# Kernel tuning notes

Hardware: AMD Instinct MI355X
Metric: run time of the kernel (lower is better)

The kernel has to match this reference:

```python
import jax, jax.numpy as jnp
import numpy as np


def setup_inputs() -> dict:
    key = jax.random.key(0)
    x = jax.random.normal(key, (32, 512, 32, 32), dtype=jnp.float32)
    return {"x": x}


def reference(x):
    B, C, H, W = x.shape
    # [B, HW, C]
    x_v = x.reshape(B, C, H * W).transpose(0, 2, 1)
    # channel means over spatial positions, detached in original (no grad path)
    x_m = jax.lax.stop_gradient(x_v.mean(axis=1))  # [B, C]
    # pairwise squared-diff score: score[b, i, j] = -(x_m[b, j] - x_m[b, i])**2
    score = -(x_m[:, None, :] - x_m[:, :, None]) ** 2  # [B, C, C]
    attn = jax.nn.softmax(score, axis=1)  # normalize over first channel axis
    # out[b, s, j] = sum_k x_v[b, s, k] * attn[b, k, j]
    out = jnp.einsum("bsk,bkj->bsj", x_v, attn)  # [B, HW, C]
    out = out.transpose(0, 2, 1).reshape(B, C, H, W)
    return jax.nn.relu(x + 0.1 * out)
```

## Files before the change

### kernel.cpp

```cpp
#include <hip/hip_runtime.h>
#include <hip/hip_bf16.h>


typedef __bf16 bf16x8 __attribute__((ext_vector_type(8)));
typedef float floatx4 __attribute__((ext_vector_type(4)));

__device__ __forceinline__ void async_cp16(const void* gsrc, void* ldst) {
    __builtin_amdgcn_global_load_lds(
        (const __attribute__((address_space(1))) unsigned int*)gsrc,
        (__attribute__((address_space(3))) unsigned int*)ldst,
        16, 0, 0);
}

__global__ __launch_bounds__(256) void mean_kernel(const float* __restrict__ x,
                                                   float* __restrict__ xm) {
    int row  = blockIdx.x * 4 + (threadIdx.x >> 6);
    int lane = threadIdx.x & 63;
    const float4* p = (const float4*)(x + (size_t)row * 1024);
    float s = 0.0f;
#pragma unroll
    for (int i = 0; i < 4; i++) {
        float4 v = p[lane + i * 64];
        s += v.x + v.y + v.z + v.w;
    }
#pragma unroll
    for (int off = 32; off; off >>= 1) s += __shfl_down(s, off);
    if (lane == 0) xm[row] = s * (1.0f / 1024.0f);
}

__global__ __launch_bounds__(256) void attn_kernel(const float* __restrict__ xm,
                                                   __bf16* __restrict__ attnT) {
    int gw   = blockIdx.x * 4 + (threadIdx.x >> 6);
    int b    = gw >> 9;
    int j    = gw & 511;
    int lane = threadIdx.x & 63;
    const float* m = xm + b * 512;
    float mj = m[j];
    float e[8];
    float s = 0.0f;
#pragma unroll
    for (int i = 0; i < 8; i++) {
        float d = mj - m[lane + i * 64];
        e[i] = __expf(-d * d);
        s += e[i];
    }
#pragma unroll
    for (int off = 32; off; off >>= 1) s += __shfl_xor(s, off);
    float inv = 1.0f / s;
    __bf16* o = attnT + (size_t)gw * 512;
#pragma unroll
    for (int i = 0; i < 8; i++) o[lane + i * 64] = (__bf16)(e[i] * inv);
}

__global__ __launch_bounds__(256, 3) void gemm_kernel(const __bf16* __restrict__ attnT,
                                                      const float* __restrict__ x,
                                                      float* __restrict__ out) {
    int b  = blockIdx.z;
    int m0 = blockIdx.y * 128;
    int n0 = blockIdx.x * 128;
    const __bf16* Ab = attnT + (size_t)b * 512 * 512 + (size_t)m0 * 512;
    const float*  xb = x + (size_t)b * 512 * 1024;

    __shared__ __bf16 As[2][128][32];
    __shared__ __bf16 Bs[128][64];

    int tid  = threadIdx.x;
    int wave = tid >> 6, lane = tid & 63;
    int wr = wave >> 1, wc = wave & 1;
    int quad = lane >> 4, l16 = lane & 15;

    int ko = tid >> 5;
    int sq = tid & 31;

    floatx4 acc[4][4];
#pragma unroll
    for (int i = 0; i < 4; i++)
#pragma unroll
        for (int j = 0; j < 4; j++) acc[i][j] = (floatx4){0.f, 0.f, 0.f, 0.f};

    for (int k0 = 0; k0 < 512; k0 += 64) {
#pragma unroll
        for (int i = 0; i < 4; i++) {
            int q = tid + i * 256;
            int ulow = q & 3, r = (q >> 2) & 127, p = q >> 9;
            async_cp16(Ab + (size_t)r * 512 + k0 + p * 32 + ulow * 8,
                       (char*)&As[0][0][0] + (size_t)q * 16);
        }
        float4 f[8];
#pragma unroll
        for (int kk = 0; kk < 8; kk++)
            f[kk] = *(const float4*)&xb[(size_t)(k0 + ko * 8 + kk) * 1024 + n0 + sq * 4];
#pragma unroll
        for (int j = 0; j < 4; j++) {
            int s = sq * 4 + j;
            bf16x8 w;
            w[0] = (__bf16)f[0].x; w[1] = (__bf16)f[1].x;
            w[2] = (__bf16)f[2].x; w[3] = (__bf16)f[3].x;
            w[4] = (__bf16)f[4].x; w[5] = (__bf16)f[5].x;
            w[6] = (__bf16)f[6].x; w[7] = (__bf16)f[7].x;
            const float* fp = (const float*)&f[0];
#pragma unroll
            for (int kk = 0; kk < 8; kk++) w[kk] = (__bf16)fp[kk * 4 + j];
            int u = ko ^ (((s >> 2) ^ s) & 7);
            *(bf16x8*)&Bs[s][u * 8] = w;
        }
        __syncthreads();
#pragma unroll
        for (int ks = 0; ks < 2; ks++) {
            bf16x8 af[4], bfv[4];
#pragma unroll
            for (int mi = 0; mi < 4; mi++)
                af[mi] = *(bf16x8*)&As[ks][wr * 64 + mi * 16 + l16][quad * 8];
#pragma unroll
            for (int ni = 0; ni < 4; ni++) {
                int n = wc * 64 + ni * 16 + l16;
                int u = (ks * 4 + quad) ^ (((n >> 2) ^ n) & 7);
                bfv[ni] = *(bf16x8*)&Bs[n][u * 8];
            }
#pragma unroll
            for (int mi = 0; mi < 4; mi++)
#pragma unroll
                for (int ni = 0; ni < 4; ni++)
                    acc[mi][ni] = __builtin_amdgcn_mfma_f32_16x16x32_bf16(
                        af[mi], bfv[ni], acc[mi][ni], 0, 0, 0);
        }
        __syncthreads();
    }

    float* ob = out + (size_t)b * 512 * 1024;
#pragma unroll
    for (int mi = 0; mi < 4; mi++)
#pragma unroll
        for (int r = 0; r < 4; r++) {
            int j = m0 + wr * 64 + mi * 16 + quad * 4 + r;
#pragma unroll
            for (int ni = 0; ni < 4; ni++) {
                int s = n0 + wc * 64 + ni * 16 + l16;
                float v = xb[(size_t)j * 1024 + s] + 0.1f * acc[mi][ni][r];
                ob[(size_t)j * 1024 + s] = fmaxf(v, 0.0f);
            }
        }
}

extern "C" void kernel_launch(void* const* d_in, const int* in_sizes, int n_in,
                              void* d_out, int out_size, void* d_ws, size_t ws_size,
                              hipStream_t stream) {
    const float* x = (const float*)d_in[0];
    float* out = (float*)d_out;
    char* ws = (char*)d_ws;
    float*  xm    = (float*)ws;
    __bf16* attnT = (__bf16*)(ws + (64 << 10));

    mean_kernel<<<4096, 256, 0, stream>>>(x, xm);
    attn_kernel<<<4096, 256, 0, stream>>>(xm, attnT);
    gemm_kernel<<<dim3(8, 4, 32), 256, 0, stream>>>(attnT, x, out);
}
```

Baseline: 158.4 us.

## Recompute softmax weights inside GEMM instead of materializing attention matrix

The attention kernel now only computes per-column inverse denominators. The GEMM recomputes exp(-(mj-mk)^2)*inv in registers to build A fragments, which removes the 16 MB bf16 attention write and its reload through LDS. The M tile shrinks from 128 to 64 with launch bounds raised to 4 blocks per CU, so twice as many blocks each re-stream x. This adds exp work per tile and doubles the reads of x.

Measured after the change: 152.9 us. 3.4% less time.

```diff
diff --git a/kernel.cpp b/kernel.cpp
--- a/kernel.cpp
+++ b/kernel.cpp
@@ -4,13 +4,6 @@
 
 typedef __bf16 bf16x8 __attribute__((ext_vector_type(8)));
 typedef float floatx4 __attribute__((ext_vector_type(4)));
-
-__device__ __forceinline__ void async_cp16(const void* gsrc, void* ldst) {
-    __builtin_amdgcn_global_load_lds(
-        (const __attribute__((address_space(1))) unsigned int*)gsrc,
-        (__attribute__((address_space(3))) unsigned int*)ldst,
-        16, 0, 0);
-}
 
 __global__ __launch_bounds__(256) void mean_kernel(const float* __restrict__ x,
                                                    float* __restrict__ xm) {
@@ -28,89 +21,94 @@
     if (lane == 0) xm[row] = s * (1.0f / 1024.0f);
 }
 
-__global__ __launch_bounds__(256) void attn_kernel(const float* __restrict__ xm,
-                                                   __bf16* __restrict__ attnT) {
+__global__ __launch_bounds__(256) void den_kernel(const float* __restrict__ xm,
+                                                  float* __restrict__ invd) {
     int gw   = blockIdx.x * 4 + (threadIdx.x >> 6);
     int b    = gw >> 9;
-    int j    = gw & 511;
     int lane = threadIdx.x & 63;
     const float* m = xm + b * 512;
-    float mj = m[j];
-    float e[8];
+    float mj = xm[gw];
     float s = 0.0f;
 #pragma unroll
     for (int i = 0; i < 8; i++) {
         float d = mj - m[lane + i * 64];
-        e[i] = __expf(-d * d);
-        s += e[i];
+        s += __expf(-d * d);
     }
 #pragma unroll
     for (int off = 32; off; off >>= 1) s += __shfl_xor(s, off);
-    float inv = 1.0f / s;
-    __bf16* o = attnT + (size_t)gw * 512;
-#pragma unroll
-    for (int i = 0; i < 8; i++) o[lane + i * 64] = (__bf16)(e[i] * inv);
+    if (lane == 0) invd[gw] = 1.0f / s;
 }
 
-__global__ __launch_bounds__(256, 3) void gemm_kernel(const __bf16* __restrict__ attnT,
+__global__ __launch_bounds__(256, 4) void gemm_kernel(const float* __restrict__ xm,
+                                                      const float* __restrict__ invd,
                                                       const float* __restrict__ x,
                                                       float* __restrict__ out) {
     int b  = blockIdx.z;
-    int m0 = blockIdx.y * 128;
+    int m0 = blockIdx.y * 64;
     int n0 = blockIdx.x * 128;
-    const __bf16* Ab = attnT + (size_t)b * 512 * 512 + (size_t)m0 * 512;
-    const float*  xb = x + (size_t)b * 512 * 1024;
+    const float* xb  = x    + (size_t)b * 512 * 1024;
+    const float* xmb = xm   + b * 512;
+    const float* ivb = invd + b * 512;
 
-    __shared__ __bf16 As[2][128][32];
     __shared__ __bf16 Bs[128][64];
 
     int tid  = threadIdx.x;
     int wave = tid >> 6, lane = tid & 63;
     int wr = wave >> 1, wc = wave & 1;
     int quad = lane >> 4, l16 = lane & 15;
-
     int ko = tid >> 5;
     int sq = tid & 31;
 
-    floatx4 acc[4][4];
+    float mjv[2], ivv[2];
 #pragma unroll
-    for (int i = 0; i < 4; i++)
+    for (int mi = 0; mi < 2; mi++) {
+        int j = m0 + wr * 32 + mi * 16 + l16;
+        mjv[mi] = xmb[j];
+        ivv[mi] = ivb[j];
+    }
+
+    floatx4 acc[2][4];
+#pragma unroll
+    for (int i = 0; i < 2; i++)
 #pragma unroll
         for (int j = 0; j < 4; j++) acc[i][j] = (floatx4){0.f, 0.f, 0.f, 0.f};
 
     for (int k0 = 0; k0 < 512; k0 += 64) {
-#pragma unroll
-        for (int i = 0; i < 4; i++) {
-            int q = tid + i * 256;
-            int ulow = q & 3, r = (q >> 2) & 127, p = q >> 9;
-            async_cp16(Ab + (size_t)r * 512 + k0 + p * 32 + ulow * 8,
-                       (char*)&As[0][0][0] + (size_t)q * 16);
-        }
         float4 f[8];
 #pragma unroll
         for (int kk = 0; kk < 8; kk++)
             f[kk] = *(const float4*)&xb[(size_t)(k0 + ko * 8 + kk) * 1024 + n0 + sq * 4];
+        const float* fp = (const float*)&f[0];
 #pragma unroll
         for (int j = 0; j < 4; j++) {
             int s = sq * 4 + j;
             bf16x8 w;
-            w[0] = (__bf16)f[0].x; w[1] = (__bf16)f[1].x;
-            w[2] = (__bf16)f[2].x; w[3] = (__bf16)f[3].x;
-            w[4] = (__bf16)f[4].x; w[5] = (__bf16)f[5].x;
-            w[6] = (__bf16)f[6].x; w[7] = (__bf16)f[7].x;
-            const float* fp = (const float*)&f[0];
 #pragma unroll
             for (int kk = 0; kk < 8; kk++) w[kk] = (__bf16)fp[kk * 4 + j];
             int u = ko ^ (((s >> 2) ^ s) & 7);
             *(bf16x8*)&Bs[s][u * 8] = w;
         }
+        bf16x8 af[2][2];
+#pragma unroll
+        for (int ks = 0; ks < 2; ks++) {
+            const float* mkp = &xmb[k0 + ks * 32 + quad * 8];
+            float4 mk0 = *(const float4*)mkp;
+            float4 mk1 = *(const float4*)(mkp + 4);
+            float mkv[8] = {mk0.x, mk0.y, mk0.z, mk0.w, mk1.x, mk1.y, mk1.z, mk1.w};
+#pragma unroll
+            for (int mi = 0; mi < 2; mi++) {
+                float mj = mjv[mi], iv = ivv[mi];
+#pragma unroll
+                for (int e = 0; e < 8; e++) {
+                    float d = mj - mkv[e];
+                    af[mi][ks][e] = (__bf16)(__expf(-d * d) * iv);
+                }
+            }
+        }
         __syncthreads();
 #pragma unroll
         for (int ks = 0; ks < 2; ks++) {
-            bf16x8 af[4], bfv[4];
-#pragma unroll
-            for (int mi = 0; mi < 4; mi++)
-                af[mi] = *(bf16x8*)&As[ks][wr * 64 + mi * 16 + l16][quad * 8];
+            bf16x8 bfv[4];
 #pragma unroll
             for (int ni = 0; ni < 4; ni++) {
                 int n = wc * 64 + ni * 16 + l16;
@@ -118,21 +116,21 @@
                 bfv[ni] = *(bf16x8*)&Bs[n][u * 8];
             }
 #pragma unroll
-            for (int mi = 0; mi < 4; mi++)
+            for (int mi = 0; mi < 2; mi++)
 #pragma unroll
                 for (int ni = 0; ni < 4; ni++)
                     acc[mi][ni] = __builtin_amdgcn_mfma_f32_16x16x32_bf16(
-                        af[mi], bfv[ni], acc[mi][ni], 0, 0, 0);
+                        af[mi][ks], bfv[ni], acc[mi][ni], 0, 0, 0);
         }
         __syncthreads();
     }
 
     float* ob = out + (size_t)b * 512 * 1024;
 #pragma unroll
-    for (int mi = 0; mi < 4; mi++)
+    for (int mi = 0; mi < 2; mi++)
 #pragma unroll
         for (int r = 0; r < 4; r++) {
-            int j = m0 + wr * 64 + mi * 16 + quad * 4 + r;
+            int j = m0 + wr * 32 + mi * 16 + quad * 4 + r;
 #pragma unroll
             for (int ni = 0; ni < 4; ni++) {
                 int s = n0 + wc * 64 + ni * 16 + l16;
@@ -148,10 +146,10 @@
     const float* x = (const float*)d_in[0];
     float* out = (float*)d_out;
     char* ws = (char*)d_ws;
-    float*  xm    = (float*)ws;
-    __bf16* attnT = (__bf16*)(ws + (64 << 10));
+    float* xm   = (float*)ws;
+    float* invd = (float*)(ws + (64 << 10));
 
     mean_kernel<<<4096, 256, 0, stream>>>(x, xm);
-    attn_kernel<<<4096, 256, 0, stream>>>(xm, attnT);
-    gemm_kernel<<<dim3(8, 4, 32), 256, 0, stream>>>(attnT, x, out);
+    den_kernel<<<4096, 256, 0, stream>>>(xm, invd);
+    gemm_kernel<<<dim3(8, 8, 32), 256, 0, stream>>>(xm, invd, x, out);
 }
```

## Drop LDS staging in GEMM; load operands directly from global into registers

Applied to the files above, without the earlier changes.

The GEMM kernel no longer stages A and B tiles through shared memory with barriers. Each wave now loads its own bf16 attention fragments and strided fp32 x values straight from global memory into MFMA registers, using a 64x256 block tile in which the four waves split the columns. Output stores become nontemporal. This removes LDS traffic and __syncthreads, but it gives up data sharing across waves: the A fragments are loaded redundantly by all four waves, and the B loads are scalar and strided across rows, which may raise global/L2 traffic.

Measured after the change: 180.4 us. +13.9%, slower.

```diff
diff --git a/kernel.cpp b/kernel.cpp
--- a/kernel.cpp
+++ b/kernel.cpp
@@ -4,13 +4,6 @@
 
 typedef __bf16 bf16x8 __attribute__((ext_vector_type(8)));
 typedef float floatx4 __attribute__((ext_vector_type(4)));
-
-__device__ __forceinline__ void async_cp16(const void* gsrc, void* ldst) {
-    __builtin_amdgcn_global_load_lds(
-        (const __attribute__((address_space(1))) unsigned int*)gsrc,
-        (__attribute__((address_space(3))) unsigned int*)ldst,
-        16, 0, 0);
-}
 
 __global__ __launch_bounds__(256) void mean_kernel(const float* __restrict__ x,
                                                    float* __restrict__ xm) {
@@ -32,10 +25,9 @@
                                                    __bf16* __restrict__ attnT) {
     int gw   = blockIdx.x * 4 + (threadIdx.x >> 6);
     int b    = gw >> 9;
-    int j    = gw & 511;
     int lane = threadIdx.x & 63;
     const float* m = xm + b * 512;
-    float mj = m[j];
+    float mj = xm[gw];
     float e[8];
     float s = 0.0f;
 #pragma unroll
@@ -56,21 +48,20 @@
                                                       const float* __restrict__ x,
                                                       float* __restrict__ out) {
     int b  = blockIdx.z;
-    int m0 = blockIdx.y * 128;
-    int n0 = blockIdx.x * 128;
-    const __bf16* Ab = attnT + (size_t)b * 512 * 512 + (size_t)m0 * 512;
-    const float*  xb = x + (size_t)b * 512 * 1024;
-
-    __shared__ __bf16 As[2][128][32];
-    __shared__ __bf16 Bs[128][64];
-
+    int m0 = blockIdx.y * 64;
+    int n0 = blockIdx.x * 256;
     int tid  = threadIdx.x;
     int wave = tid >> 6, lane = tid & 63;
-    int wr = wave >> 1, wc = wave & 1;
     int quad = lane >> 4, l16 = lane & 15;
 
-    int ko = tid >> 5;
-    int sq = tid & 31;
+    const __bf16* Ab = attnT + (size_t)b * 512 * 512;
+    const float*  xb = x + (size_t)b * 512 * 1024;
+    int col = n0 + wave * 64 + l16;
+
+    const __bf16* ap[4];
+#pragma unroll
+    for (int mi = 0; mi < 4; mi++)
+        ap[mi] = Ab + (size_t)(m0 + mi * 16 + l16) * 512 + quad * 8;
 
     floatx4 acc[4][4];
 #pragma unroll
@@ -78,53 +69,31 @@
 #pragma unroll
         for (int j = 0; j < 4; j++) acc[i][j] = (floatx4){0.f, 0.f, 0.f, 0.f};
 
-    for (int k0 = 0; k0 < 512; k0 += 64) {
+    for (int k0 = 0; k0 < 512; k0 += 32) {
+        bf16x8 af[4];
 #pragma unroll
-        for (int i = 0; i < 4; i++) {
-            int q = tid + i * 256;
-            int ulow = q & 3, r = (q >> 2) & 127, p = q >> 9;
-            async_cp16(Ab + (size_t)r * 512 + k0 + p * 32 + ulow * 8,
-                       (char*)&As[0][0][0] + (size_t)q * 16);
-        }
-        float4 f[8];
+        for (int mi = 0; mi < 4; mi++) af[mi] = *(const bf16x8*)(ap[mi] + k0);
+
+        const float* bp = xb + (size_t)(k0 + quad * 8) * 1024 + col;
+        float t[4][8];
 #pragma unroll
-        for (int kk = 0; kk < 8; kk++)
-            f[kk] = *(const float4*)&xb[(size_t)(k0 + ko * 8 + kk) * 1024 + n0 + sq * 4];
+        for (int ni = 0; ni < 4; ni++)
 #pragma unroll
-        for (int j = 0; j < 4; j++) {
-            int s = sq * 4 + j;
-            bf16x8 w;
-            w[0] = (__bf16)f[0].x; w[1] = (__bf16)f[1].x;
-            w[2] = (__bf16)f[2].x; w[3] = (__bf16)f[3].x;
-            w[4] = (__bf16)f[4].x; w[5] = (__bf16)f[5].x;
-            w[6] = (__bf16)f[6].x; w[7] = (__bf16)f[7].x;
-            const float* fp = (const float*)&f[0];
+            for (int e = 0; e < 8; e++)
+                t[ni][e] = bp[(size_t)e * 1024 + ni * 16];
+
+        bf16x8 bfv[4];
 #pragma unroll
-            for (int kk = 0; kk < 8; kk++) w[kk] = (__bf16)fp[kk * 4 + j];
-            int u = ko ^ (((s >> 2) ^ s) & 7);
-            *(bf16x8*)&Bs[s][u * 8] = w;
-        }
-        __syncthreads();
+        for (int ni = 0; ni < 4; ni++)
 #pragma unroll
-        for (int ks = 0; ks < 2; ks++) {
-            bf16x8 af[4], bfv[4];
+            for (int e = 0; e < 8; e++) bfv[ni][e] = (__bf16)t[ni][e];
+
+#pragma unroll
+        for (int ni = 0; ni < 4; ni++)
 #pragma unroll
             for (int mi = 0; mi < 4; mi++)
-                af[mi] = *(bf16x8*)&As[ks][wr * 64 + mi * 16 + l16][quad * 8];
-#pragma unroll
-            for (int ni = 0; ni < 4; ni++) {
-                int n = wc * 64 + ni * 16 + l16;
-                int u = (ks * 4 + quad) ^ (((n >> 2) ^ n) & 7);
-                bfv[ni] = *(bf16x8*)&Bs[n][u * 8];
-            }
-#pragma unroll
-            for (int mi = 0; mi < 4; mi++)
-#pragma unroll
-                for (int ni = 0; ni < 4; ni++)
-                    acc[mi][ni] = __builtin_amdgcn_mfma_f32_16x16x32_bf16(
-                        af[mi], bfv[ni], acc[mi][ni], 0, 0, 0);
-        }
-        __syncthreads();
+                acc[mi][ni] = __builtin_amdgcn_mfma_f32_16x16x32_bf16(
+                    af[mi], bfv[ni], acc[mi][ni], 0, 0, 0);
     }
 
     float* ob = out + (size_t)b * 512 * 1024;
@@ -132,12 +101,13 @@
     for (int mi = 0; mi < 4; mi++)
 #pragma unroll
         for (int r = 0; r < 4; r++) {
-            int j = m0 + wr * 64 + mi * 16 + quad * 4 + r;
+            int j = m0 + mi * 16 + quad * 4 + r;
+            const float* xr = xb + (size_t)j * 1024;
+            float* orow = ob + (size_t)j * 1024;
 #pragma unroll
             for (int ni = 0; ni < 4; ni++) {
-                int s = n0 + wc * 64 + ni * 16 + l16;
-                float v = xb[(size_t)j * 1024 + s] + 0.1f * acc[mi][ni][r];
-                ob[(size_t)j * 1024 + s] = fmaxf(v, 0.0f);
+                float v = xr[col + ni * 16] + 0.1f * acc[mi][ni][r];
+                __builtin_nontemporal_store(fmaxf(v, 0.0f), &orow[col + ni * 16]);
             }
         }
 }
@@ -153,5 +123,5 @@
 
     mean_kernel<<<4096, 256, 0, stream>>>(x, xm);
     attn_kernel<<<4096, 256, 0, stream>>>(xm, attnT);
-    gemm_kernel<<<dim3(8, 4, 32), 256, 0, stream>>>(attnT, x, out);
+    gemm_kernel<<<dim3(4, 8, 32), 256, 0, stream>>>(attnT, x, out);
 }
```

## Double-buffer B tile in LDS and load A fragments directly from global

Applied to the files above, without the earlier changes.

The GEMM kernel no longer stages the attention matrix A through LDS. Each wave reads its bf16 A fragments straight from global memory, which is likely served from cache because the matrix is small. The converted x tile B is now double-buffered in LDS, so the next tile is staged while MFMAs run on the current one, removing one barrier per iteration. The trade-off is more global load latency inside the MFMA loop and doubled LDS for B. The attn kernel also indexes the mean directly.

Result: slower. 179.1 us (+13.1%).

```diff
diff --git a/kernel.cpp b/kernel.cpp
--- a/kernel.cpp
+++ b/kernel.cpp
@@ -4,13 +4,6 @@
 
 typedef __bf16 bf16x8 __attribute__((ext_vector_type(8)));
 typedef float floatx4 __attribute__((ext_vector_type(4)));
-
-__device__ __forceinline__ void async_cp16(const void* gsrc, void* ldst) {
-    __builtin_amdgcn_global_load_lds(
-        (const __attribute__((address_space(1))) unsigned int*)gsrc,
-        (__attribute__((address_space(3))) unsigned int*)ldst,
-        16, 0, 0);
-}
 
 __global__ __launch_bounds__(256) void mean_kernel(const float* __restrict__ x,
                                                    float* __restrict__ xm) {
@@ -32,10 +25,9 @@
                                                    __bf16* __restrict__ attnT) {
     int gw   = blockIdx.x * 4 + (threadIdx.x >> 6);
     int b    = gw >> 9;
-    int j    = gw & 511;
     int lane = threadIdx.x & 63;
     const float* m = xm + b * 512;
-    float mj = m[j];
+    float mj = xm[gw];
     float e[8];
     float s = 0.0f;
 #pragma unroll
@@ -58,19 +50,22 @@
     int b  = blockIdx.z;
     int m0 = blockIdx.y * 128;
     int n0 = blockIdx.x * 128;
-    const __bf16* Ab = attnT + (size_t)b * 512 * 512 + (size_t)m0 * 512;
+    const __bf16* Ab = attnT + (size_t)b * 512 * 512;
     const float*  xb = x + (size_t)b * 512 * 1024;
 
-    __shared__ __bf16 As[2][128][32];
-    __shared__ __bf16 Bs[128][64];
+    __shared__ __bf16 Bs[2][128][64];
 
     int tid  = threadIdx.x;
     int wave = tid >> 6, lane = tid & 63;
     int wr = wave >> 1, wc = wave & 1;
     int quad = lane >> 4, l16 = lane & 15;
-
     int ko = tid >> 5;
     int sq = tid & 31;
+
+    const __bf16* ap[4];
+#pragma unroll
+    for (int mi = 0; mi < 4; mi++)
+        ap[mi] = Ab + (size_t)(m0 + wr * 64 + mi * 16 + l16) * 512 + quad * 8;
 
     floatx4 acc[4][4];
 #pragma unroll
@@ -78,44 +73,39 @@
 #pragma unroll
         for (int j = 0; j < 4; j++) acc[i][j] = (floatx4){0.f, 0.f, 0.f, 0.f};
 
-    for (int k0 = 0; k0 < 512; k0 += 64) {
-#pragma unroll
-        for (int i = 0; i < 4; i++) {
-            int q = tid + i * 256;
-            int ulow = q & 3, r = (q >> 2) & 127, p = q >> 9;
-            async_cp16(Ab + (size_t)r * 512 + k0 + p * 32 + ulow * 8,
-                       (char*)&As[0][0][0] + (size_t)q * 16);
-        }
+    auto stage = [&](int k0, int buf) {
         float4 f[8];
 #pragma unroll
         for (int kk = 0; kk < 8; kk++)
             f[kk] = *(const float4*)&xb[(size_t)(k0 + ko * 8 + kk) * 1024 + n0 + sq * 4];
+        const float* fp = (const float*)&f[0];
 #pragma unroll
         for (int j = 0; j < 4; j++) {
             int s = sq * 4 + j;
             bf16x8 w;
-            w[0] = (__bf16)f[0].x; w[1] = (__bf16)f[1].x;
-            w[2] = (__bf16)f[2].x; w[3] = (__bf16)f[3].x;
-            w[4] = (__bf16)f[4].x; w[5] = (__bf16)f[5].x;
-            w[6] = (__bf16)f[6].x; w[7] = (__bf16)f[7].x;
-            const float* fp = (const float*)&f[0];
 #pragma unroll
             for (int kk = 0; kk < 8; kk++) w[kk] = (__bf16)fp[kk * 4 + j];
             int u = ko ^ (((s >> 2) ^ s) & 7);
-            *(bf16x8*)&Bs[s][u * 8] = w;
+            *(bf16x8*)&Bs[buf][s][u * 8] = w;
         }
+    };
+
+    stage(0, 0);
+    int buf = 0;
+    for (int k0 = 0; k0 < 512; k0 += 64) {
         __syncthreads();
+        if (k0 + 64 < 512) stage(k0 + 64, buf ^ 1);
 #pragma unroll
         for (int ks = 0; ks < 2; ks++) {
             bf16x8 af[4], bfv[4];
 #pragma unroll
             for (int mi = 0; mi < 4; mi++)
-                af[mi] = *(bf16x8*)&As[ks][wr * 64 + mi * 16 + l16][quad * 8];
+                af[mi] = *(const bf16x8*)(ap[mi] + k0 + ks * 32);
 #pragma unroll
             for (int ni = 0; ni < 4; ni++) {
                 int n = wc * 64 + ni * 16 + l16;
                 int u = (ks * 4 + quad) ^ (((n >> 2) ^ n) & 7);
-                bfv[ni] = *(bf16x8*)&Bs[n][u * 8];
+                bfv[ni] = *(bf16x8*)&Bs[buf][n][u * 8];
             }
 #pragma unroll
             for (int mi = 0; mi < 4; mi++)
@@ -124,7 +114,7 @@
                     acc[mi][ni] = __builtin_amdgcn_mfma_f32_16x16x32_bf16(
                         af[mi], bfv[ni], acc[mi][ni], 0, 0, 0);
         }
-        __syncthreads();
+        buf ^= 1;
     }
 
     float* ob = out + (size_t)b * 512 * 1024;
@@ -133,11 +123,13 @@
 #pragma unroll
         for (int r = 0; r < 4; r++) {
             int j = m0 + wr * 64 + mi * 16 + quad * 4 + r;
+            const float* xr = xb + (size_t)j * 1024;
+            float* orow = ob + (size_t)j * 1024;
 #pragma unroll
             for (int ni = 0; ni < 4; ni++) {
                 int s = n0 + wc * 64 + ni * 16 + l16;
-                float v = xb[(size_t)j * 1024 + s] + 0.1f * acc[mi][ni][r];
-                ob[(size_t)j * 1024 + s] = fmaxf(v, 0.0f);
+                float v = xr[s] + 0.1f * acc[mi][ni][r];
+                orow[s] = fmaxf(v, 0.0f);
             }
         }
 }
```
